# Kernel tuning notes

Measured on AMD Instinct MI355X. Metric: run time of the kernel, lower is better.

## Reference

```python
import jax, jax.numpy as jnp
import numpy as np

MEMORY_LENGTH = 32   # past states remembered
N_TARGETS = 3        # leak sources
T_STEPS = 1000       # duration / dt
DT = 0.1
HIDDEN = 128         # policy MLP hidden width
N_AGENTS = 1024      # vmapped batch of rollouts
IN_DIM = MEMORY_LENGTH * 3 + MEMORY_LENGTH  # flattened x_hist + conc_hist


def setup_inputs() -> dict:
    key = jax.random.key(0)
    k0, k1, k2, k3, k4 = jax.random.split(key, 5)
    target_pos = jax.random.normal(k0, (N_TARGETS, 2), dtype=jnp.float32) * 5.0
    logsigma = jax.random.normal(k1, (N_TARGETS,), dtype=jnp.float32) * 0.5
    x_inits = jax.random.normal(k2, (N_AGENTS, 3), dtype=jnp.float32) * 2.0
    W1 = jax.random.normal(k3, (HIDDEN, IN_DIM), dtype=jnp.float32) / np.sqrt(IN_DIM).astype(np.float32)
    b1 = jnp.zeros((HIDDEN,), dtype=jnp.float32)
    W2 = jax.random.normal(k4, (2, HIDDEN), dtype=jnp.float32) / np.sqrt(HIDDEN).astype(np.float32)
    b2 = jnp.zeros((2,), dtype=jnp.float32)
    return {"target_pos": target_pos, "logsigma": logsigma, "x_inits": x_inits,
            "W1": W1, "b1": b1, "W2": W2, "b2": b2}


def _concentration(x, y, target_pos, sigma):
    # x, y: [N]; target_pos: [nt, 2]; sigma: [nt] -> conc: [N]
    d2 = (x[:, None] - target_pos[None, :, 0]) ** 2 + (y[:, None] - target_pos[None, :, 1]) ** 2
    return ((1.0 / sigma) * jnp.exp(-d2 / sigma)).sum(-1)


def reference(target_pos, logsigma, x_inits, W1, b1, W2, b2):
    sigma = jnp.exp(logsigma)
    N = x_inits.shape[0]
    # initial histories: memory_length copies of the initial state / concentration
    x_hist0 = jnp.tile(x_inits[:, None, :], (1, MEMORY_LENGTH, 1))        # [N, M, 3]
    conc0 = _concentration(x_inits[:, 0], x_inits[:, 1], target_pos, sigma)
    conc_hist0 = jnp.tile(conc0[:, None], (1, MEMORY_LENGTH))             # [N, M]

    def step(carry, _):
        x_hist, conc_hist, x_cur = carry
        # policy MLP on flattened histories -> tanh controls (v, omega)
        feats = jnp.concatenate([x_hist.reshape(N, -1), conc_hist], axis=-1)  # [N, 4M]
        h = jax.nn.relu(feats @ W1.T + b1)
        u = jnp.tanh(h @ W2.T + b2)                                            # [N, 2]
        v, w = u[:, 0], u[:, 1]
        th = x_cur[:, 2]
        # Dubins car dynamics (zero actuation noise)
        x_next = x_cur + DT * jnp.stack([v * jnp.cos(th), v * jnp.sin(th), w], axis=-1)
        # shift histories: drop oldest, insert newest at front
        x_hist = jnp.concatenate([x_next[:, None, :], x_hist[:, :-1, :]], axis=1)
        c = _concentration(x_next[:, 0], x_next[:, 1], target_pos, sigma)
        conc_hist = jnp.concatenate([c[:, None], conc_hist[:, :-1]], axis=1)
        return (x_hist, conc_hist, x_next), (x_next, u)

    _, (traj, ctrl) = jax.lax.scan(step, (x_hist0, conc_hist0, x_inits), None, length=T_STEPS)
    # traj: [T, N, 3], ctrl: [T, N, 2]
    d2 = ((traj[:, :, 0][..., None] - target_pos[None, None, :, 0]) ** 2
          + (traj[:, :, 1][..., None] - target_pos[None, None, :, 1]) ** 2)   # [T, N, nt]
    per_target = (-1.0 / sigma) * jnp.exp(-d2 / sigma)                        # [T, N, nt]
    cost = per_target.mean(axis=(0, 1)).sum() + (ctrl ** 2).mean()
    return cost
```

## Files before the change

kernel.cpp:

```cpp
#include <hip/hip_runtime.h>

#define T_STEPS 1000
#define DT 0.1f
#define HIDDEN 128
#define N_AGENTS 1024

typedef float v2f __attribute__((ext_vector_type(2)));

__device__ __forceinline__ float tanh_fast(float x) {
    float e = __expf(2.0f * x);
    return 1.0f - 2.0f * __builtin_amdgcn_rcpf(e + 1.0f);
}

__device__ __forceinline__ v2f opaque_load8(const float* p) {
    v2f v;
    asm volatile("global_load_dwordx2 %0, %1, off\n\ts_waitcnt vmcnt(0)"
                 : "=v"(v)
                 : "v"((unsigned long long)(uintptr_t)p)
                 : "memory");
    return v;
}

__device__ __forceinline__ float uniformf(float v) {
    return __builtin_bit_cast(float,
        __builtin_amdgcn_readfirstlane(__builtin_bit_cast(int, v)));
}

__device__ __forceinline__ void wave_sum2_dpp(float& a, float& b) {
    asm volatile(
        "s_nop 1\n\t"
        "v_add_f32_dpp %0, %0, %0 row_shr:1 row_mask:0xf bank_mask:0xf bound_ctrl:0\n\t"
        "v_add_f32_dpp %1, %1, %1 row_shr:1 row_mask:0xf bank_mask:0xf bound_ctrl:0\n\t"
        "s_nop 0\n\t"
        "v_add_f32_dpp %0, %0, %0 row_shr:2 row_mask:0xf bank_mask:0xf bound_ctrl:0\n\t"
        "v_add_f32_dpp %1, %1, %1 row_shr:2 row_mask:0xf bank_mask:0xf bound_ctrl:0\n\t"
        "s_nop 0\n\t"
        "v_add_f32_dpp %0, %0, %0 row_shr:4 row_mask:0xf bank_mask:0xf bound_ctrl:0\n\t"
        "v_add_f32_dpp %1, %1, %1 row_shr:4 row_mask:0xf bank_mask:0xf bound_ctrl:0\n\t"
        "s_nop 0\n\t"
        "v_add_f32_dpp %0, %0, %0 row_shr:8 row_mask:0xf bank_mask:0xf bound_ctrl:0\n\t"
        "v_add_f32_dpp %1, %1, %1 row_shr:8 row_mask:0xf bank_mask:0xf bound_ctrl:0\n\t"
        "s_nop 0\n\t"
        "v_add_f32_dpp %0, %0, %0 row_bcast:15 row_mask:0xa bank_mask:0xf bound_ctrl:0\n\t"
        "v_add_f32_dpp %1, %1, %1 row_bcast:15 row_mask:0xa bank_mask:0xf bound_ctrl:0\n\t"
        "s_nop 0\n\t"
        "v_add_f32_dpp %0, %0, %0 row_bcast:31 row_mask:0xc bank_mask:0xf bound_ctrl:0\n\t"
        "v_add_f32_dpp %1, %1, %1 row_bcast:31 row_mask:0xc bank_mask:0xf bound_ctrl:0\n\t"
        "s_nop 1"
        : "+v"(a), "+v"(b));
}

__global__ void pack_kernel(const float* __restrict__ W1,
                            float* __restrict__ pw) {
    const int row = blockIdx.x;
    const int a   = threadIdx.x;
    const float* rp = W1 + row * 128;
    float* out = pw + row * 128;
    out[2*a]          = rp[3*a];
    out[2*a + 1]      = rp[3*a + 1];
    out[64 + 2*a]     = rp[3*a + 2];
    out[64 + 2*a + 1] = rp[96 + a];
}

__global__ __launch_bounds__(128)
__attribute__((amdgpu_waves_per_eu(2, 2)))
void sim_kernel(const float* __restrict__ target_pos,
                const float* __restrict__ logsigma,
                const float* __restrict__ x_inits,
                const float* __restrict__ pw,
                const float* __restrict__ b1,
                const float* __restrict__ W2,
                const float* __restrict__ b2,
                float2* __restrict__ ws) {
    const int agent = blockIdx.x;
    const int tid  = threadIdx.x;
    const int h    = tid >> 6;
    const int lane = tid & 63;
    const int rowA = lane;
    const int rowB = lane + 64;

    __shared__ float2 part1[32][64];
    __shared__ float4 e4buf[16];

    if (h == 0) __builtin_amdgcn_s_setprio(1);

    const float tx0 = uniformf(target_pos[0]), ty0 = uniformf(target_pos[1]);
    const float tx1 = uniformf(target_pos[2]), ty1 = uniformf(target_pos[3]);
    const float tx2 = uniformf(target_pos[4]), ty2 = uniformf(target_pos[5]);
    const float is0 = uniformf(1.0f / expf(logsigma[0]));
    const float is1 = uniformf(1.0f / expf(logsigma[1]));
    const float is2 = uniformf(1.0f / expf(logsigma[2]));

    v2f WxyA[16], WzcA[16], WxyB[16], WzcB[16];
    {
        const float* baseA = pw + rowA * 128;
        const float* baseB = pw + rowB * 128;
        #pragma unroll
        for (int i = 0; i < 16; ++i) {
            WxyA[i] = opaque_load8(baseA + 32 * h + 2 * i);
            WzcA[i] = opaque_load8(baseA + 64 + 32 * h + 2 * i);
            WxyB[i] = opaque_load8(baseB + 32 * h + 2 * i);
            WzcB[i] = opaque_load8(baseB + 64 + 32 * h + 2 * i);
        }
    }
    const float b1A = b1[rowA], b1B = b1[rowB];
    const float w20A = W2[rowA], w20B = W2[rowB];
    const float w21A = W2[HIDDEN + rowA], w21B = W2[HIDDEN + rowB];
    const float b2x = uniformf(b2[0]), b2y = uniformf(b2[1]);

    auto conc = [&](float px, float py) {
        float dx0 = px - tx0, dy0 = py - ty0;
        float dx1 = px - tx1, dy1 = py - ty1;
        float dx2 = px - tx2, dy2 = py - ty2;
        float cc  = is0 * __expf(-(dx0*dx0 + dy0*dy0) * is0);
        cc       += is1 * __expf(-(dx1*dx1 + dy1*dy1) * is1);
        cc       += is2 * __expf(-(dx2*dx2 + dy2*dy2) * is2);
        return cc;
    };

    float x  = uniformf(x_inits[3 * agent]);
    float y  = uniformf(x_inits[3 * agent + 1]);
    float th = uniformf(x_inits[3 * agent + 2]);
    float c  = conc(x, y);

    if (h == 0) {
        v2f RA[16], RB[16];
        {
            v2f exy0 = {x, y}, ezc0 = {th, c};
            v2f aA = {0.f,0.f}, aB = {0.f,0.f};
            #pragma unroll
            for (int k = 15; k >= 0; --k) {
                aA = WxyA[k]*exy0 + aA;  aA = WzcA[k]*ezc0 + aA;
                aB = WxyB[k]*exy0 + aB;  aB = WzcB[k]*ezc0 + aB;
                RA[k] = aA;  RB[k] = aB;
            }
            if (lane == 0) {
                float4 e0 = make_float4(x, y, th, c);
                #pragma unroll
                for (int m = 9; m < 16; ++m) e4buf[m] = e0;
                e4buf[0] = e0;
            }
        }
        __syncthreads();
        float2 pl = part1[0][lane];
        v2f es_xy[4], es_zc[4];
        float S_c = 0.f, S_u = 0.f;

        auto h0_step = [&](int j, int s16) {
            float hA = fmaxf((RA[j].x + RA[j].y) + pl.x + b1A, 0.f);
            float hB = fmaxf((RB[j].x + RB[j].y) + pl.y + b1B, 0.f);
            float r0 = fmaf(w20A, hA, w20B * hB);
            float r1 = fmaf(w21A, hA, w21B * hB);
            wave_sum2_dpp(r0, r1);
            float s0 = __builtin_bit_cast(float,
                __builtin_amdgcn_readlane(__builtin_bit_cast(int, r0), 63));
            float s1 = __builtin_bit_cast(float,
                __builtin_amdgcn_readlane(__builtin_bit_cast(int, r1), 63));
            float v  = tanh_fast(s0 + b2x);
            float wv = tanh_fast(s1 + b2y);
            S_u += v * v + wv * wv;
            float sn = __sinf(th), cs = __cosf(th);
            float dv = DT * v;
            x  = fmaf(dv, cs, x);
            y  = fmaf(dv, sn, y);
            th = fmaf(DT, wv, th);
            c  = conc(x, y);
            S_c += c;
            if (lane == 0) e4buf[(j + 1) & 15] = make_float4(x, y, th, c);
            v2f exy = {x, y}, ezc = {th, c};
            es_xy[j & 3] = exy;  es_zc[j & 3] = ezc;
            #pragma unroll
            for (int k = 0; k < 3; ++k) {
                if (k <= 2 - (j & 3)) {
                    const int m = (j + 1 + k) & 15;
                    RA[m] = WxyA[k]*exy + RA[m];  RA[m] = WzcA[k]*ezc + RA[m];
                    RB[m] = WxyB[k]*exy + RB[m];  RB[m] = WzcB[k]*ezc + RB[m];
                }
            }
            pl = part1[(s16 + j + 1) & 31][lane];
        };
        auto h0_batch = [&](int q) {
            #pragma unroll
            for (int kk = 0; kk < 16; ++kk) {
                #pragma unroll
                for (int i = 0; i < 4; ++i) {
                    if (kk >= 3 - i) {
                        const int m = (4*q + i + 1 + kk) & 15;
                        if (i == 3 && kk >= 12) {
                            RA[m] = WxyA[kk]*es_xy[i];
                            RA[m] = WzcA[kk]*es_zc[i] + RA[m];
                            RB[m] = WxyB[kk]*es_xy[i];
                            RB[m] = WzcB[kk]*es_zc[i] + RB[m];
                        } else {
                            RA[m] = WxyA[kk]*es_xy[i] + RA[m];
                            RA[m] = WzcA[kk]*es_zc[i] + RA[m];
                            RB[m] = WxyB[kk]*es_xy[i] + RB[m];
                            RB[m] = WzcB[kk]*es_zc[i] + RB[m];
                        }
                    }
                }
            }
        };

        #pragma unroll 1
        for (int b = 0; b < 62; ++b) {
            const int s16 = (b & 1) << 4;
            __syncthreads();
            #pragma unroll
            for (int j = 0; j < 4; ++j) h0_step(j, s16);
            h0_batch(0);
            #pragma unroll
            for (int j = 4; j < 8; ++j) h0_step(j, s16);
            h0_batch(1);
            __syncthreads();
            #pragma unroll
            for (int j = 8; j < 12; ++j) h0_step(j, s16);
            h0_batch(2);
            #pragma unroll
            for (int j = 12; j < 16; ++j) h0_step(j, s16);
            h0_batch(3);
        }
        __syncthreads();
        #pragma unroll
        for (int j = 0; j < 4; ++j) h0_step(j, 0);
        h0_batch(0);
        #pragma unroll
        for (int j = 4; j < 8; ++j) h0_step(j, 0);

        if (lane == 0) ws[agent] = make_float2(S_c, S_u);
    } else {
        v2f PA[20], PB[20];
        {
            v2f exy0 = {x, y}, ezc0 = {th, c};
            #pragma unroll
            for (int i = 15; i < 20; ++i) { PA[i] = (v2f){0.f,0.f}; PB[i] = (v2f){0.f,0.f}; }
            v2f aA = {0.f,0.f}, aB = {0.f,0.f};
            #pragma unroll
            for (int k = 15; k >= 1; --k) {
                aA = WxyA[k]*exy0 + aA;  aA = WzcA[k]*ezc0 + aA;
                aB = WxyB[k]*exy0 + aB;  aB = WzcB[k]*ezc0 + aB;
                PA[k-1] = aA;  PB[k-1] = aB;
            }
            v2f fA = WxyA[0]*exy0 + aA;  fA = WzcA[0]*ezc0 + fA;
            v2f fB = WxyB[0]*exy0 + aB;  fB = WzcB[0]*ezc0 + fB;
            float2 full = make_float2(fA.x + fA.y, fB.x + fB.y);
            #pragma unroll
            for (int s = 0; s <= 8; ++s) part1[s][lane] = full;
        }
        __syncthreads();

        auto h1_batch = [&](int n, int b1w) {
            v2f pxy[4], pzc[4];
            #pragma unroll
            for (int i = 0; i < 4; ++i) {
                float4 e = e4buf[(9 + 4*n + i) & 15];
                pxy[i] = (v2f){e.x, e.y};
                pzc[i] = (v2f){e.z, e.w};
            }
            #pragma unroll
            for (int kk = 0; kk < 16; ++kk) {
                #pragma unroll
                for (int i = 0; i < 4; ++i) {
                    const int idx = i + kk;
                    PA[idx] = WxyA[kk]*pxy[i] + PA[idx];
                    PA[idx] = WzcA[kk]*pzc[i] + PA[idx];
                    PB[idx] = WxyB[kk]*pxy[i] + PB[idx];
                    PB[idx] = WzcB[kk]*pzc[i] + PB[idx];
                }
            }
            #pragma unroll
            for (int i = 0; i < 4; ++i) {
                part1[(b1w * 16 + 9 + 4*n + i) & 31][lane] =
                    make_float2(PA[i].x + PA[i].y, PB[i].x + PB[i].y);
            }
            #pragma unroll
            for (int i = 0; i < 16; ++i) { PA[i] = PA[i+4]; PB[i] = PB[i+4]; }
            #pragma unroll
            for (int i = 16; i < 20; ++i) { PA[i] = (v2f){0.f,0.f}; PB[i] = (v2f){0.f,0.f}; }
        };

        #pragma unroll 1
        for (int b = 0; b < 62; ++b) {
            const int b1w = b & 1;
            __syncthreads();
            h1_batch(0, b1w);
            h1_batch(1, b1w);
            __syncthreads();
            h1_batch(2, b1w);
            h1_batch(3, b1w);
        }
        __syncthreads();
    }
}

__global__ void reduce_kernel(const float2* __restrict__ ws,
                              float* __restrict__ out) {
    const int tid = threadIdx.x;
    float sc = 0.f, su = 0.f;
    for (int i = tid; i < N_AGENTS; i += 256) {
        float2 v = ws[i];
        sc += v.x;
        su += v.y;
    }
    #pragma unroll
    for (int off = 32; off > 0; off >>= 1) {
        sc += __shfl_xor(sc, off);
        su += __shfl_xor(su, off);
    }
    __shared__ float2 partw[4];
    int wave = tid >> 6;
    if ((tid & 63) == 0) partw[wave] = make_float2(sc, su);
    __syncthreads();
    if (tid == 0) {
        float SC = partw[0].x + partw[1].x + partw[2].x + partw[3].x;
        float SU = partw[0].y + partw[1].y + partw[2].y + partw[3].y;
        const float invNT  = 1.0f / (float)(N_AGENTS * T_STEPS);
        const float invNT2 = 1.0f / (float)(N_AGENTS * T_STEPS * 2);
        out[0] = -SC * invNT + SU * invNT2;
    }
}

extern "C" void kernel_launch(void* const* d_in, const int* in_sizes, int n_in,
                              void* d_out, int out_size, void* d_ws, size_t ws_size,
                              hipStream_t stream) {
    const float* target_pos = (const float*)d_in[0];
    const float* logsigma   = (const float*)d_in[1];
    const float* x_inits    = (const float*)d_in[2];
    const float* W1         = (const float*)d_in[3];
    const float* b1         = (const float*)d_in[4];
    const float* W2         = (const float*)d_in[5];
    const float* b2         = (const float*)d_in[6];

    float*  pw   = (float*)d_ws;
    float2* sums = (float2*)((char*)d_ws + 64 * 1024);

    pack_kernel<<<HIDDEN, 32, 0, stream>>>(W1, pw);
    sim_kernel<<<N_AGENTS, 128, 0, stream>>>(target_pos, logsigma, x_inits,
                                             pw, b1, W2, b2, sums);
    reduce_kernel<<<1, 256, 0, stream>>>(sums, (float*)d_out);
}
```

Baseline: 632.3 us.

## Merge two-wave producer/consumer split into a single wave per agent

Collapses the two cooperating waves per agent (one stepping dynamics, one precomputing older-history partial sums through LDS with barriers) into one 64-thread wave. That wave holds all W1 columns in registers and interleaves the older-history partial-sum batches between dynamics step groups, using register arrays and double-buffered state vectors. This removes the LDS traffic and __syncthreads barriers on the critical loop. In exchange the serial chain per wave gets longer, since the batch work no longer overlaps, and register pressure roughly doubles (128 v2f weights), which risks spills.

```diff
diff --git a/kernel.cpp b/kernel.cpp
--- a/kernel.cpp
+++ b/kernel.cpp
@@ -62,8 +62,8 @@
     out[64 + 2*a + 1] = rp[96 + a];
 }
 
-__global__ __launch_bounds__(128)
-__attribute__((amdgpu_waves_per_eu(2, 2)))
+__global__ __launch_bounds__(64)
+__attribute__((amdgpu_waves_per_eu(1, 1)))
 void sim_kernel(const float* __restrict__ target_pos,
                 const float* __restrict__ logsigma,
                 const float* __restrict__ x_inits,
@@ -73,16 +73,9 @@
                 const float* __restrict__ b2,
                 float2* __restrict__ ws) {
     const int agent = blockIdx.x;
-    const int tid  = threadIdx.x;
-    const int h    = tid >> 6;
-    const int lane = tid & 63;
+    const int lane  = threadIdx.x;
     const int rowA = lane;
     const int rowB = lane + 64;
-
-    __shared__ float2 part1[32][64];
-    __shared__ float4 e4buf[16];
-
-    if (h == 0) __builtin_amdgcn_s_setprio(1);
 
     const float tx0 = uniformf(target_pos[0]), ty0 = uniformf(target_pos[1]);
     const float tx1 = uniformf(target_pos[2]), ty1 = uniformf(target_pos[3]);
@@ -91,16 +84,16 @@
     const float is1 = uniformf(1.0f / expf(logsigma[1]));
     const float is2 = uniformf(1.0f / expf(logsigma[2]));
 
-    v2f WxyA[16], WzcA[16], WxyB[16], WzcB[16];
+    v2f WxyA[32], WzcA[32], WxyB[32], WzcB[32];
     {
         const float* baseA = pw + rowA * 128;
         const float* baseB = pw + rowB * 128;
         #pragma unroll
-        for (int i = 0; i < 16; ++i) {
-            WxyA[i] = opaque_load8(baseA + 32 * h + 2 * i);
-            WzcA[i] = opaque_load8(baseA + 64 + 32 * h + 2 * i);
-            WxyB[i] = opaque_load8(baseB + 32 * h + 2 * i);
-            WzcB[i] = opaque_load8(baseB + 64 + 32 * h + 2 * i);
+        for (int i = 0; i < 32; ++i) {
+            WxyA[i] = opaque_load8(baseA + 2 * i);
+            WzcA[i] = opaque_load8(baseA + 64 + 2 * i);
+            WxyB[i] = opaque_load8(baseB + 2 * i);
+            WzcB[i] = opaque_load8(baseB + 64 + 2 * i);
         }
     }
     const float b1A = b1[rowA], b1B = b1[rowB];
@@ -123,174 +116,152 @@
     float th = uniformf(x_inits[3 * agent + 2]);
     float c  = conc(x, y);
 
-    if (h == 0) {
-        v2f RA[16], RB[16];
-        {
-            v2f exy0 = {x, y}, ezc0 = {th, c};
-            v2f aA = {0.f,0.f}, aB = {0.f,0.f};
+    v2f RA[16], RB[16];
+    v2f PA[20], PB[20];
+    float plA[16], plB[16];
+    v2f eA_xy[4], eA_zc[4];
+    v2f eB_xy[4], eB_zc[4];
+    float S_c = 0.f, S_u = 0.f;
+
+    {
+        v2f exy0 = {x, y}, ezc0 = {th, c};
+        {   v2f aA = {0.f,0.f}, aB = {0.f,0.f};
             #pragma unroll
             for (int k = 15; k >= 0; --k) {
                 aA = WxyA[k]*exy0 + aA;  aA = WzcA[k]*ezc0 + aA;
                 aB = WxyB[k]*exy0 + aB;  aB = WzcB[k]*ezc0 + aB;
                 RA[k] = aA;  RB[k] = aB;
             }
-            if (lane == 0) {
-                float4 e0 = make_float4(x, y, th, c);
-                #pragma unroll
-                for (int m = 9; m < 16; ++m) e4buf[m] = e0;
-                e4buf[0] = e0;
-            }
-        }
-        __syncthreads();
-        float2 pl = part1[0][lane];
-        v2f es_xy[4], es_zc[4];
-        float S_c = 0.f, S_u = 0.f;
-
-        auto h0_step = [&](int j, int s16) {
-            float hA = fmaxf((RA[j].x + RA[j].y) + pl.x + b1A, 0.f);
-            float hB = fmaxf((RB[j].x + RB[j].y) + pl.y + b1B, 0.f);
-            float r0 = fmaf(w20A, hA, w20B * hB);
-            float r1 = fmaf(w21A, hA, w21B * hB);
-            wave_sum2_dpp(r0, r1);
-            float s0 = __builtin_bit_cast(float,
-                __builtin_amdgcn_readlane(__builtin_bit_cast(int, r0), 63));
-            float s1 = __builtin_bit_cast(float,
-                __builtin_amdgcn_readlane(__builtin_bit_cast(int, r1), 63));
-            float v  = tanh_fast(s0 + b2x);
-            float wv = tanh_fast(s1 + b2y);
-            S_u += v * v + wv * wv;
-            float sn = __sinf(th), cs = __cosf(th);
-            float dv = DT * v;
-            x  = fmaf(dv, cs, x);
-            y  = fmaf(dv, sn, y);
-            th = fmaf(DT, wv, th);
-            c  = conc(x, y);
-            S_c += c;
-            if (lane == 0) e4buf[(j + 1) & 15] = make_float4(x, y, th, c);
-            v2f exy = {x, y}, ezc = {th, c};
-            es_xy[j & 3] = exy;  es_zc[j & 3] = ezc;
-            #pragma unroll
-            for (int k = 0; k < 3; ++k) {
-                if (k <= 2 - (j & 3)) {
-                    const int m = (j + 1 + k) & 15;
-                    RA[m] = WxyA[k]*exy + RA[m];  RA[m] = WzcA[k]*ezc + RA[m];
-                    RB[m] = WxyB[k]*exy + RB[m];  RB[m] = WzcB[k]*ezc + RB[m];
+        }
+        #pragma unroll
+        for (int i = 15; i < 20; ++i) { PA[i] = (v2f){0.f,0.f}; PB[i] = (v2f){0.f,0.f}; }
+        {   v2f aA = {0.f,0.f}, aB = {0.f,0.f};
+            #pragma unroll
+            for (int k = 15; k >= 1; --k) {
+                aA = WxyA[16+k]*exy0 + aA;  aA = WzcA[16+k]*ezc0 + aA;
+                aB = WxyB[16+k]*exy0 + aB;  aB = WzcB[16+k]*ezc0 + aB;
+                PA[k-1] = aA;  PB[k-1] = aB;
+            }
+            v2f fA = WxyA[16]*exy0 + aA;  fA = WzcA[16]*ezc0 + fA;
+            v2f fB = WxyB[16]*exy0 + aB;  fB = WzcB[16]*ezc0 + fB;
+            float fullA = fA.x + fA.y, fullB = fB.x + fB.y;
+            #pragma unroll
+            for (int s = 0; s <= 8; ++s) { plA[s] = fullA; plB[s] = fullB; }
+        }
+        #pragma unroll
+        for (int i = 0; i < 4; ++i) { eB_xy[i] = exy0; eB_zc[i] = ezc0; }
+    }
+
+    auto h1_batch = [&](v2f (&px)[4], v2f (&pz)[4], int n) {
+        #pragma unroll
+        for (int kk = 0; kk < 16; ++kk) {
+            #pragma unroll
+            for (int i = 0; i < 4; ++i) {
+                const int idx = i + kk;
+                if (i == 3 && kk >= 12) {
+                    PA[idx] = WxyA[16+kk]*px[i];
+                    PA[idx] = WzcA[16+kk]*pz[i] + PA[idx];
+                    PB[idx] = WxyB[16+kk]*px[i];
+                    PB[idx] = WzcB[16+kk]*pz[i] + PB[idx];
+                } else {
+                    PA[idx] = WxyA[16+kk]*px[i] + PA[idx];
+                    PA[idx] = WzcA[16+kk]*pz[i] + PA[idx];
+                    PB[idx] = WxyB[16+kk]*px[i] + PB[idx];
+                    PB[idx] = WzcB[16+kk]*pz[i] + PB[idx];
                 }
             }
-            pl = part1[(s16 + j + 1) & 31][lane];
-        };
-        auto h0_batch = [&](int q) {
-            #pragma unroll
-            for (int kk = 0; kk < 16; ++kk) {
-                #pragma unroll
-                for (int i = 0; i < 4; ++i) {
-                    if (kk >= 3 - i) {
-                        const int m = (4*q + i + 1 + kk) & 15;
-                        if (i == 3 && kk >= 12) {
-                            RA[m] = WxyA[kk]*es_xy[i];
-                            RA[m] = WzcA[kk]*es_zc[i] + RA[m];
-                            RB[m] = WxyB[kk]*es_xy[i];
-                            RB[m] = WzcB[kk]*es_zc[i] + RB[m];
-                        } else {
-                            RA[m] = WxyA[kk]*es_xy[i] + RA[m];
-                            RA[m] = WzcA[kk]*es_zc[i] + RA[m];
-                            RB[m] = WxyB[kk]*es_xy[i] + RB[m];
-                            RB[m] = WzcB[kk]*es_zc[i] + RB[m];
-                        }
+        }
+        #pragma unroll
+        for (int i = 0; i < 4; ++i) {
+            plA[(9 + 4*n + i) & 15] = PA[i].x + PA[i].y;
+            plB[(9 + 4*n + i) & 15] = PB[i].x + PB[i].y;
+        }
+        #pragma unroll
+        for (int i = 0; i < 16; ++i) { PA[i] = PA[i+4]; PB[i] = PB[i+4]; }
+    };
+
+    h1_batch(eB_xy, eB_zc, 0);
+
+    auto h0_step = [&](int j, v2f (&bx)[4], v2f (&bz)[4]) {
+        float hA = fmaxf((RA[j & 15].x + RA[j & 15].y) + plA[j & 15] + b1A, 0.f);
+        float hB = fmaxf((RB[j & 15].x + RB[j & 15].y) + plB[j & 15] + b1B, 0.f);
+        float r0 = fmaf(w20A, hA, w20B * hB);
+        float r1 = fmaf(w21A, hA, w21B * hB);
+        wave_sum2_dpp(r0, r1);
+        float s0 = __builtin_bit_cast(float,
+            __builtin_amdgcn_readlane(__builtin_bit_cast(int, r0), 63));
+        float s1 = __builtin_bit_cast(float,
+            __builtin_amdgcn_readlane(__builtin_bit_cast(int, r1), 63));
+        float v  = tanh_fast(s0 + b2x);
+        float wv = tanh_fast(s1 + b2y);
+        S_u += v * v + wv * wv;
+        float sn = __sinf(th), cs = __cosf(th);
+        float dv = DT * v;
+        x  = fmaf(dv, cs, x);
+        y  = fmaf(dv, sn, y);
+        th = fmaf(DT, wv, th);
+        c  = conc(x, y);
+        S_c += c;
+        v2f exy = {x, y}, ezc = {th, c};
+        bx[j & 3] = exy;  bz[j & 3] = ezc;
+        #pragma unroll
+        for (int k = 0; k < 3; ++k) {
+            if (k <= 2 - (j & 3)) {
+                const int m = (j + 1 + k) & 15;
+                RA[m] = WxyA[k]*exy + RA[m];  RA[m] = WzcA[k]*ezc + RA[m];
+                RB[m] = WxyB[k]*exy + RB[m];  RB[m] = WzcB[k]*ezc + RB[m];
+            }
+        }
+    };
+    auto h0_batch = [&](int q, v2f (&bx)[4], v2f (&bz)[4]) {
+        #pragma unroll
+        for (int kk = 0; kk < 16; ++kk) {
+            #pragma unroll
+            for (int i = 0; i < 4; ++i) {
+                if (kk >= 3 - i) {
+                    const int m = (4*q + i + 1 + kk) & 15;
+                    if (i == 3 && kk >= 12) {
+                        RA[m] = WxyA[kk]*bx[i];
+                        RA[m] = WzcA[kk]*bz[i] + RA[m];
+                        RB[m] = WxyB[kk]*bx[i];
+                        RB[m] = WzcB[kk]*bz[i] + RB[m];
+                    } else {
+                        RA[m] = WxyA[kk]*bx[i] + RA[m];
+                        RA[m] = WzcA[kk]*bz[i] + RA[m];
+                        RB[m] = WxyB[kk]*bx[i] + RB[m];
+                        RB[m] = WzcB[kk]*bz[i] + RB[m];
                     }
                 }
             }
-        };
-
-        #pragma unroll 1
-        for (int b = 0; b < 62; ++b) {
-            const int s16 = (b & 1) << 4;
-            __syncthreads();
-            #pragma unroll
-            for (int j = 0; j < 4; ++j) h0_step(j, s16);
-            h0_batch(0);
-            #pragma unroll
-            for (int j = 4; j < 8; ++j) h0_step(j, s16);
-            h0_batch(1);
-            __syncthreads();
-            #pragma unroll
-            for (int j = 8; j < 12; ++j) h0_step(j, s16);
-            h0_batch(2);
-            #pragma unroll
-            for (int j = 12; j < 16; ++j) h0_step(j, s16);
-            h0_batch(3);
-        }
-        __syncthreads();
-        #pragma unroll
-        for (int j = 0; j < 4; ++j) h0_step(j, 0);
-        h0_batch(0);
-        #pragma unroll
-        for (int j = 4; j < 8; ++j) h0_step(j, 0);
-
-        if (lane == 0) ws[agent] = make_float2(S_c, S_u);
-    } else {
-        v2f PA[20], PB[20];
-        {
-            v2f exy0 = {x, y}, ezc0 = {th, c};
-            #pragma unroll
-            for (int i = 15; i < 20; ++i) { PA[i] = (v2f){0.f,0.f}; PB[i] = (v2f){0.f,0.f}; }
-            v2f aA = {0.f,0.f}, aB = {0.f,0.f};
-            #pragma unroll
-            for (int k = 15; k >= 1; --k) {
-                aA = WxyA[k]*exy0 + aA;  aA = WzcA[k]*ezc0 + aA;
-                aB = WxyB[k]*exy0 + aB;  aB = WzcB[k]*ezc0 + aB;
-                PA[k-1] = aA;  PB[k-1] = aB;
-            }
-            v2f fA = WxyA[0]*exy0 + aA;  fA = WzcA[0]*ezc0 + fA;
-            v2f fB = WxyB[0]*exy0 + aB;  fB = WzcB[0]*ezc0 + fB;
-            float2 full = make_float2(fA.x + fA.y, fB.x + fB.y);
-            #pragma unroll
-            for (int s = 0; s <= 8; ++s) part1[s][lane] = full;
-        }
-        __syncthreads();
-
-        auto h1_batch = [&](int n, int b1w) {
-            v2f pxy[4], pzc[4];
-            #pragma unroll
-            for (int i = 0; i < 4; ++i) {
-                float4 e = e4buf[(9 + 4*n + i) & 15];
-                pxy[i] = (v2f){e.x, e.y};
-                pzc[i] = (v2f){e.z, e.w};
-            }
-            #pragma unroll
-            for (int kk = 0; kk < 16; ++kk) {
-                #pragma unroll
-                for (int i = 0; i < 4; ++i) {
-                    const int idx = i + kk;
-                    PA[idx] = WxyA[kk]*pxy[i] + PA[idx];
-                    PA[idx] = WzcA[kk]*pzc[i] + PA[idx];
-                    PB[idx] = WxyB[kk]*pxy[i] + PB[idx];
-                    PB[idx] = WzcB[kk]*pzc[i] + PB[idx];
-                }
-            }
-            #pragma unroll
-            for (int i = 0; i < 4; ++i) {
-                part1[(b1w * 16 + 9 + 4*n + i) & 31][lane] =
-                    make_float2(PA[i].x + PA[i].y, PB[i].x + PB[i].y);
-            }
-            #pragma unroll
-            for (int i = 0; i < 16; ++i) { PA[i] = PA[i+4]; PB[i] = PB[i+4]; }
-            #pragma unroll
-            for (int i = 16; i < 20; ++i) { PA[i] = (v2f){0.f,0.f}; PB[i] = (v2f){0.f,0.f}; }
-        };
-
-        #pragma unroll 1
-        for (int b = 0; b < 62; ++b) {
-            const int b1w = b & 1;
-            __syncthreads();
-            h1_batch(0, b1w);
-            h1_batch(1, b1w);
-            __syncthreads();
-            h1_batch(2, b1w);
-            h1_batch(3, b1w);
-        }
-        __syncthreads();
-    }
+        }
+    };
+
+    #pragma unroll 1
+    for (int b = 0; b < 62; ++b) {
+        h0_step(0, eA_xy, eA_zc);  h0_step(1, eA_xy, eA_zc);
+        h0_step(2, eA_xy, eA_zc);  h0_step(3, eA_xy, eA_zc);
+        h0_batch(0, eA_xy, eA_zc);
+        h1_batch(eB_xy, eB_zc, 1);
+        h0_step(4, eB_xy, eB_zc);  h0_step(5, eB_xy, eB_zc);
+        h0_step(6, eB_xy, eB_zc);  h0_step(7, eB_xy, eB_zc);
+        h0_batch(1, eB_xy, eB_zc);
+        h1_batch(eA_xy, eA_zc, 2);
+        h0_step(8, eA_xy, eA_zc);   h0_step(9, eA_xy, eA_zc);
+        h0_step(10, eA_xy, eA_zc);  h0_step(11, eA_xy, eA_zc);
+        h0_batch(2, eA_xy, eA_zc);
+        h1_batch(eB_xy, eB_zc, 3);
+        h0_step(12, eB_xy, eB_zc);  h0_step(13, eB_xy, eB_zc);
+        h0_step(14, eB_xy, eB_zc);  h0_step(15, eB_xy, eB_zc);
+        h0_batch(3, eB_xy, eB_zc);
+        h1_batch(eA_xy, eA_zc, 0);
+    }
+    h0_step(0, eA_xy, eA_zc);  h0_step(1, eA_xy, eA_zc);
+    h0_step(2, eA_xy, eA_zc);  h0_step(3, eA_xy, eA_zc);
+    h0_batch(0, eA_xy, eA_zc);
+    h0_step(4, eB_xy, eB_zc);  h0_step(5, eB_xy, eB_zc);
+    h0_step(6, eB_xy, eB_zc);  h0_step(7, eB_xy, eB_zc);
+
+    if (lane == 0) ws[agent] = make_float2(S_c, S_u);
 }
 
 __global__ void reduce_kernel(const float2* __restrict__ ws,
@@ -335,7 +306,7 @@
     float2* sums = (float2*)((char*)d_ws + 64 * 1024);
 
     pack_kernel<<<HIDDEN, 32, 0, stream>>>(W1, pw);
-    sim_kernel<<<N_AGENTS, 128, 0, stream>>>(target_pos, logsigma, x_inits,
-                                             pw, b1, W2, b2, sums);
+    sim_kernel<<<N_AGENTS, 64, 0, stream>>>(target_pos, logsigma, x_inits,
+                                            pw, b1, W2, b2, sums);
     reduce_kernel<<<1, 256, 0, stream>>>(sums, (float*)d_out);
 }
```

After: 1.792 ms. 2.83x slower.

## Process two agents per block with weights in AGPRs to interleave serial chains

Applied to the files above, without the earlier changes.

Each block now simulates two agents instead of one. The dependent per-step chains (the DPP reduction, tanh, dynamics and concentration) of the two agents are interleaved, hiding their latency, and the weight reads are amortized over both. Weights move into accumulation registers via v_accvgpr_write/read to make room for the doubled accumulator state, and occupancy is set to one wave per EU. Smaller changes: the DPP reduction is widened to four values without the s_nop padding, sin/cos is computed one step ahead, and history writes are batched. The risks are extra accvgpr read traffic, register pressure, and half as many blocks on a 256-CU part.

```diff
diff --git a/kernel.cpp b/kernel.cpp
--- a/kernel.cpp
+++ b/kernel.cpp
@@ -8,7 +8,7 @@
 typedef float v2f __attribute__((ext_vector_type(2)));
 
 __device__ __forceinline__ float tanh_fast(float x) {
-    float e = __expf(2.0f * x);
+    float e = __builtin_amdgcn_exp2f(x * 0x1.715476p+1f);
     return 1.0f - 2.0f * __builtin_amdgcn_rcpf(e + 1.0f);
 }
 
@@ -21,33 +21,52 @@
     return v;
 }
 
+__device__ __forceinline__ void awrite(float& ax, float& ay, v2f v) {
+    asm("v_accvgpr_write_b32 %0, %2\n\tv_accvgpr_write_b32 %1, %3"
+        : "=a"(ax), "=a"(ay) : "v"(v.x), "v"(v.y));
+}
+__device__ __forceinline__ v2f aread(const float& ax, const float& ay) {
+    float rx, ry;
+    asm("v_accvgpr_read_b32 %0, %2\n\tv_accvgpr_read_b32 %1, %3"
+        : "=v"(rx), "=v"(ry) : "a"(ax), "a"(ay));
+    return (v2f){rx, ry};
+}
+
 __device__ __forceinline__ float uniformf(float v) {
     return __builtin_bit_cast(float,
         __builtin_amdgcn_readfirstlane(__builtin_bit_cast(int, v)));
 }
 
-__device__ __forceinline__ void wave_sum2_dpp(float& a, float& b) {
+__device__ __forceinline__ void wave_sum4_dpp(float& a, float& b,
+                                              float& c, float& d) {
     asm volatile(
         "s_nop 1\n\t"
         "v_add_f32_dpp %0, %0, %0 row_shr:1 row_mask:0xf bank_mask:0xf bound_ctrl:0\n\t"
         "v_add_f32_dpp %1, %1, %1 row_shr:1 row_mask:0xf bank_mask:0xf bound_ctrl:0\n\t"
-        "s_nop 0\n\t"
+        "v_add_f32_dpp %2, %2, %2 row_shr:1 row_mask:0xf bank_mask:0xf bound_ctrl:0\n\t"
+        "v_add_f32_dpp %3, %3, %3 row_shr:1 row_mask:0xf bank_mask:0xf bound_ctrl:0\n\t"
         "v_add_f32_dpp %0, %0, %0 row_shr:2 row_mask:0xf bank_mask:0xf bound_ctrl:0\n\t"
         "v_add_f32_dpp %1, %1, %1 row_shr:2 row_mask:0xf bank_mask:0xf bound_ctrl:0\n\t"
-        "s_nop 0\n\t"
+        "v_add_f32_dpp %2, %2, %2 row_shr:2 row_mask:0xf bank_mask:0xf bound_ctrl:0\n\t"
+        "v_add_f32_dpp %3, %3, %3 row_shr:2 row_mask:0xf bank_mask:0xf bound_ctrl:0\n\t"
         "v_add_f32_dpp %0, %0, %0 row_shr:4 row_mask:0xf bank_mask:0xf bound_ctrl:0\n\t"
         "v_add_f32_dpp %1, %1, %1 row_shr:4 row_mask:0xf bank_mask:0xf bound_ctrl:0\n\t"
-        "s_nop 0\n\t"
+        "v_add_f32_dpp %2, %2, %2 row_shr:4 row_mask:0xf bank_mask:0xf bound_ctrl:0\n\t"
+        "v_add_f32_dpp %3, %3, %3 row_shr:4 row_mask:0xf bank_mask:0xf bound_ctrl:0\n\t"
         "v_add_f32_dpp %0, %0, %0 row_shr:8 row_mask:0xf bank_mask:0xf bound_ctrl:0\n\t"
         "v_add_f32_dpp %1, %1, %1 row_shr:8 row_mask:0xf bank_mask:0xf bound_ctrl:0\n\t"
-        "s_nop 0\n\t"
+        "v_add_f32_dpp %2, %2, %2 row_shr:8 row_mask:0xf bank_mask:0xf bound_ctrl:0\n\t"
+        "v_add_f32_dpp %3, %3, %3 row_shr:8 row_mask:0xf bank_mask:0xf bound_ctrl:0\n\t"
         "v_add_f32_dpp %0, %0, %0 row_bcast:15 row_mask:0xa bank_mask:0xf bound_ctrl:0\n\t"
         "v_add_f32_dpp %1, %1, %1 row_bcast:15 row_mask:0xa bank_mask:0xf bound_ctrl:0\n\t"
-        "s_nop 0\n\t"
+        "v_add_f32_dpp %2, %2, %2 row_bcast:15 row_mask:0xa bank_mask:0xf bound_ctrl:0\n\t"
+        "v_add_f32_dpp %3, %3, %3 row_bcast:15 row_mask:0xa bank_mask:0xf bound_ctrl:0\n\t"
         "v_add_f32_dpp %0, %0, %0 row_bcast:31 row_mask:0xc bank_mask:0xf bound_ctrl:0\n\t"
         "v_add_f32_dpp %1, %1, %1 row_bcast:31 row_mask:0xc bank_mask:0xf bound_ctrl:0\n\t"
+        "v_add_f32_dpp %2, %2, %2 row_bcast:31 row_mask:0xc bank_mask:0xf bound_ctrl:0\n\t"
+        "v_add_f32_dpp %3, %3, %3 row_bcast:31 row_mask:0xc bank_mask:0xf bound_ctrl:0\n\t"
         "s_nop 1"
-        : "+v"(a), "+v"(b));
+        : "+v"(a), "+v"(b), "+v"(c), "+v"(d));
 }
 
 __global__ void pack_kernel(const float* __restrict__ W1,
@@ -63,7 +82,7 @@
 }
 
 __global__ __launch_bounds__(128)
-__attribute__((amdgpu_waves_per_eu(2, 2)))
+__attribute__((amdgpu_waves_per_eu(1, 1)))
 void sim_kernel(const float* __restrict__ target_pos,
                 const float* __restrict__ logsigma,
                 const float* __restrict__ x_inits,
@@ -72,15 +91,15 @@
                 const float* __restrict__ W2,
                 const float* __restrict__ b2,
                 float2* __restrict__ ws) {
-    const int agent = blockIdx.x;
+    const int blk  = blockIdx.x;
     const int tid  = threadIdx.x;
     const int h    = tid >> 6;
     const int lane = tid & 63;
     const int rowA = lane;
     const int rowB = lane + 64;
 
-    __shared__ float2 part1[32][64];
-    __shared__ float4 e4buf[16];
+    __shared__ float2 part1[2][32][64];
+    __shared__ float4 e4buf[2][16];
 
     if (h == 0) __builtin_amdgcn_s_setprio(1);
 
@@ -91,18 +110,24 @@
     const float is1 = uniformf(1.0f / expf(logsigma[1]));
     const float is2 = uniformf(1.0f / expf(logsigma[2]));
 
-    v2f WxyA[16], WzcA[16], WxyB[16], WzcB[16];
+    float WxAx[16], WxAy[16], WzAx[16], WzAy[16];
+    float WxBx[16], WxBy[16], WzBx[16], WzBy[16];
     {
         const float* baseA = pw + rowA * 128;
         const float* baseB = pw + rowB * 128;
         #pragma unroll
         for (int i = 0; i < 16; ++i) {
-            WxyA[i] = opaque_load8(baseA + 32 * h + 2 * i);
-            WzcA[i] = opaque_load8(baseA + 64 + 32 * h + 2 * i);
-            WxyB[i] = opaque_load8(baseB + 32 * h + 2 * i);
-            WzcB[i] = opaque_load8(baseB + 64 + 32 * h + 2 * i);
-        }
-    }
+            awrite(WxAx[i], WxAy[i], opaque_load8(baseA + 32*h + 2*i));
+            awrite(WzAx[i], WzAy[i], opaque_load8(baseA + 64 + 32*h + 2*i));
+            awrite(WxBx[i], WxBy[i], opaque_load8(baseB + 32*h + 2*i));
+            awrite(WzBx[i], WzBy[i], opaque_load8(baseB + 64 + 32*h + 2*i));
+        }
+    }
+    #define WXA(k) aread(WxAx[k], WxAy[k])
+    #define WZA(k) aread(WzAx[k], WzAy[k])
+    #define WXB(k) aread(WxBx[k], WxBy[k])
+    #define WZB(k) aread(WzBx[k], WzBy[k])
+
     const float b1A = b1[rowA], b1B = b1[rowB];
     const float w20A = W2[rowA], w20B = W2[rowB];
     const float w21A = W2[HIDDEN + rowA], w21B = W2[HIDDEN + rowB];
@@ -118,84 +143,140 @@
         return cc;
     };
 
-    float x  = uniformf(x_inits[3 * agent]);
-    float y  = uniformf(x_inits[3 * agent + 1]);
-    float th = uniformf(x_inits[3 * agent + 2]);
-    float c  = conc(x, y);
+    float x[2], y[2], th[2], c[2];
+    #pragma unroll
+    for (int ag = 0; ag < 2; ++ag) {
+        const int agent = 2*blk + ag;
+        x[ag]  = uniformf(x_inits[3*agent]);
+        y[ag]  = uniformf(x_inits[3*agent + 1]);
+        th[ag] = uniformf(x_inits[3*agent + 2]);
+        c[ag]  = conc(x[ag], y[ag]);
+    }
 
     if (h == 0) {
-        v2f RA[16], RB[16];
+        v2f RA[2][16], RB[2][16];
         {
-            v2f exy0 = {x, y}, ezc0 = {th, c};
-            v2f aA = {0.f,0.f}, aB = {0.f,0.f};
+            v2f exy0[2], ezc0[2], aA[2], aB[2];
+            #pragma unroll
+            for (int ag = 0; ag < 2; ++ag) {
+                exy0[ag] = (v2f){x[ag], y[ag]};
+                ezc0[ag] = (v2f){th[ag], c[ag]};
+                aA[ag] = (v2f){0.f,0.f};  aB[ag] = (v2f){0.f,0.f};
+            }
             #pragma unroll
             for (int k = 15; k >= 0; --k) {
-                aA = WxyA[k]*exy0 + aA;  aA = WzcA[k]*ezc0 + aA;
-                aB = WxyB[k]*exy0 + aB;  aB = WzcB[k]*ezc0 + aB;
-                RA[k] = aA;  RB[k] = aB;
+                v2f wxa = WXA(k), wza = WZA(k);
+                v2f wxb = WXB(k), wzb = WZB(k);
+                #pragma unroll
+                for (int ag = 0; ag < 2; ++ag) {
+                    aA[ag] = wxa*exy0[ag] + aA[ag];  aA[ag] = wza*ezc0[ag] + aA[ag];
+                    aB[ag] = wxb*exy0[ag] + aB[ag];  aB[ag] = wzb*ezc0[ag] + aB[ag];
+                    RA[ag][k] = aA[ag];  RB[ag][k] = aB[ag];
+                }
             }
             if (lane == 0) {
-                float4 e0 = make_float4(x, y, th, c);
-                #pragma unroll
-                for (int m = 9; m < 16; ++m) e4buf[m] = e0;
-                e4buf[0] = e0;
-            }
-        }
+                #pragma unroll
+                for (int ag = 0; ag < 2; ++ag) {
+                    float4 e0 = make_float4(x[ag], y[ag], th[ag], c[ag]);
+                    #pragma unroll
+                    for (int m = 9; m < 16; ++m) e4buf[ag][m] = e0;
+                    e4buf[ag][0] = e0;
+                }
+            }
+        }
+        float sn[2], cs[2];
+        #pragma unroll
+        for (int ag = 0; ag < 2; ++ag) { sn[ag] = __sinf(th[ag]); cs[ag] = __cosf(th[ag]); }
         __syncthreads();
-        float2 pl = part1[0][lane];
-        v2f es_xy[4], es_zc[4];
-        float S_c = 0.f, S_u = 0.f;
+        float2 pl[2];
+        #pragma unroll
+        for (int ag = 0; ag < 2; ++ag) pl[ag] = part1[ag][0][lane];
+        v2f es_xy[2][4], es_zc[2][4];
+        float S_c[2] = {0.f, 0.f}, S_u[2] = {0.f, 0.f};
 
         auto h0_step = [&](int j, int s16) {
-            float hA = fmaxf((RA[j].x + RA[j].y) + pl.x + b1A, 0.f);
-            float hB = fmaxf((RB[j].x + RB[j].y) + pl.y + b1B, 0.f);
-            float r0 = fmaf(w20A, hA, w20B * hB);
-            float r1 = fmaf(w21A, hA, w21B * hB);
-            wave_sum2_dpp(r0, r1);
-            float s0 = __builtin_bit_cast(float,
-                __builtin_amdgcn_readlane(__builtin_bit_cast(int, r0), 63));
-            float s1 = __builtin_bit_cast(float,
-                __builtin_amdgcn_readlane(__builtin_bit_cast(int, r1), 63));
-            float v  = tanh_fast(s0 + b2x);
-            float wv = tanh_fast(s1 + b2y);
-            S_u += v * v + wv * wv;
-            float sn = __sinf(th), cs = __cosf(th);
-            float dv = DT * v;
-            x  = fmaf(dv, cs, x);
-            y  = fmaf(dv, sn, y);
-            th = fmaf(DT, wv, th);
-            c  = conc(x, y);
-            S_c += c;
-            if (lane == 0) e4buf[(j + 1) & 15] = make_float4(x, y, th, c);
-            v2f exy = {x, y}, ezc = {th, c};
-            es_xy[j & 3] = exy;  es_zc[j & 3] = ezc;
+            float r0[2], r1[2];
+            #pragma unroll
+            for (int ag = 0; ag < 2; ++ag) {
+                float hA = fmaxf((RA[ag][j].x + RA[ag][j].y) + pl[ag].x + b1A, 0.f);
+                float hB = fmaxf((RB[ag][j].x + RB[ag][j].y) + pl[ag].y + b1B, 0.f);
+                r0[ag] = fmaf(w20A, hA, w20B * hB);
+                r1[ag] = fmaf(w21A, hA, w21B * hB);
+            }
+            wave_sum4_dpp(r0[0], r1[0], r0[1], r1[1]);
+            #pragma unroll
+            for (int ag = 0; ag < 2; ++ag) {
+                float s0 = __builtin_bit_cast(float,
+                    __builtin_amdgcn_readlane(__builtin_bit_cast(int, r0[ag]), 63));
+                float s1 = __builtin_bit_cast(float,
+                    __builtin_amdgcn_readlane(__builtin_bit_cast(int, r1[ag]), 63));
+                float v  = tanh_fast(s0 + b2x);
+                float wv = tanh_fast(s1 + b2y);
+                S_u[ag] += v * v + wv * wv;
+                float dv = DT * v;
+                x[ag]  = fmaf(dv, cs[ag], x[ag]);
+                y[ag]  = fmaf(dv, sn[ag], y[ag]);
+                th[ag] = fmaf(DT, wv, th[ag]);
+                sn[ag] = __sinf(th[ag]);  cs[ag] = __cosf(th[ag]);
+                c[ag]  = conc(x[ag], y[ag]);
+                S_c[ag] += c[ag];
+                es_xy[ag][j & 3] = (v2f){x[ag], y[ag]};
+                es_zc[ag][j & 3] = (v2f){th[ag], c[ag]};
+            }
             #pragma unroll
             for (int k = 0; k < 3; ++k) {
                 if (k <= 2 - (j & 3)) {
                     const int m = (j + 1 + k) & 15;
-                    RA[m] = WxyA[k]*exy + RA[m];  RA[m] = WzcA[k]*ezc + RA[m];
-                    RB[m] = WxyB[k]*exy + RB[m];  RB[m] = WzcB[k]*ezc + RB[m];
-                }
-            }
-            pl = part1[(s16 + j + 1) & 31][lane];
+                    v2f wxa = WXA(k), wza = WZA(k);
+                    v2f wxb = WXB(k), wzb = WZB(k);
+                    #pragma unroll
+                    for (int ag = 0; ag < 2; ++ag) {
+                        RA[ag][m] = wxa*es_xy[ag][j & 3] + RA[ag][m];
+                        RA[ag][m] = wza*es_zc[ag][j & 3] + RA[ag][m];
+                        RB[ag][m] = wxb*es_xy[ag][j & 3] + RB[ag][m];
+                        RB[ag][m] = wzb*es_zc[ag][j & 3] + RB[ag][m];
+                    }
+                }
+            }
+            #pragma unroll
+            for (int ag = 0; ag < 2; ++ag)
+                pl[ag] = part1[ag][(s16 + j + 1) & 31][lane];
+        };
+        auto h0_flush = [&](int g) {
+            if (lane == 0) {
+                #pragma unroll
+                for (int ag = 0; ag < 2; ++ag) {
+                    #pragma unroll
+                    for (int i = 0; i < 4; ++i) {
+                        e4buf[ag][(4*g + 1 + i) & 15] =
+                            make_float4(es_xy[ag][i].x, es_xy[ag][i].y,
+                                        es_zc[ag][i].x, es_zc[ag][i].y);
+                    }
+                }
+            }
         };
         auto h0_batch = [&](int q) {
             #pragma unroll
             for (int kk = 0; kk < 16; ++kk) {
+                v2f wxa = WXA(kk), wza = WZA(kk);
+                v2f wxb = WXB(kk), wzb = WZB(kk);
                 #pragma unroll
                 for (int i = 0; i < 4; ++i) {
                     if (kk >= 3 - i) {
                         const int m = (4*q + i + 1 + kk) & 15;
-                        if (i == 3 && kk >= 12) {
-                            RA[m] = WxyA[kk]*es_xy[i];
-                            RA[m] = WzcA[kk]*es_zc[i] + RA[m];
-                            RB[m] = WxyB[kk]*es_xy[i];
-                            RB[m] = WzcB[kk]*es_zc[i] + RB[m];
-                        } else {
-                            RA[m] = WxyA[kk]*es_xy[i] + RA[m];
-                            RA[m] = WzcA[kk]*es_zc[i] + RA[m];
-                            RB[m] = WxyB[kk]*es_xy[i] + RB[m];
-                            RB[m] = WzcB[kk]*es_zc[i] + RB[m];
+                        #pragma unroll
+                        for (int ag = 0; ag < 2; ++ag) {
+                            if (i == 3 && kk >= 12) {
+                                RA[ag][m] = wxa*es_xy[ag][i];
+                                RA[ag][m] = wza*es_zc[ag][i] + RA[ag][m];
+                                RB[ag][m] = wxb*es_xy[ag][i];
+                                RB[ag][m] = wzb*es_zc[ag][i] + RB[ag][m];
+                            } else {
+                                RA[ag][m] = wxa*es_xy[ag][i] + RA[ag][m];
+                                RA[ag][m] = wza*es_zc[ag][i] + RA[ag][m];
+                                RB[ag][m] = wxb*es_xy[ag][i] + RB[ag][m];
+                                RB[ag][m] = wzb*es_zc[ag][i] + RB[ag][m];
+                            }
                         }
                     }
                 }
@@ -206,77 +287,121 @@
         for (int b = 0; b < 62; ++b) {
             const int s16 = (b & 1) << 4;
             __syncthreads();
-            #pragma unroll
-            for (int j = 0; j < 4; ++j) h0_step(j, s16);
+            h0_step(0, s16);  h0_step(1, s16);
+            h0_step(2, s16);  h0_step(3, s16);
+            h0_flush(0);
             h0_batch(0);
-            #pragma unroll
-            for (int j = 4; j < 8; ++j) h0_step(j, s16);
+            h0_step(4, s16);  h0_step(5, s16);
+            h0_step(6, s16);  h0_step(7, s16);
+            h0_flush(1);
             h0_batch(1);
             __syncthreads();
-            #pragma unroll
-            for (int j = 8; j < 12; ++j) h0_step(j, s16);
+            h0_step(8, s16);   h0_step(9, s16);
+            h0_step(10, s16);  h0_step(11, s16);
+            h0_flush(2);
             h0_batch(2);
-            #pragma unroll
-            for (int j = 12; j < 16; ++j) h0_step(j, s16);
+            h0_step(12, s16);  h0_step(13, s16);
+            h0_step(14, s16);  h0_step(15, s16);
+            h0_flush(3);
             h0_batch(3);
         }
         __syncthreads();
-        #pragma unroll
-        for (int j = 0; j < 4; ++j) h0_step(j, 0);
+        h0_step(0, 0);  h0_step(1, 0);
+        h0_step(2, 0);  h0_step(3, 0);
+        h0_flush(0);
         h0_batch(0);
-        #pragma unroll
-        for (int j = 4; j < 8; ++j) h0_step(j, 0);
-
-        if (lane == 0) ws[agent] = make_float2(S_c, S_u);
+        h0_step(4, 0);  h0_step(5, 0);
+        h0_step(6, 0);  h0_step(7, 0);
+
+        if (lane == 0) {
+            ws[2*blk]     = make_float2(S_c[0], S_u[0]);
+            ws[2*blk + 1] = make_float2(S_c[1], S_u[1]);
+        }
     } else {
-        v2f PA[20], PB[20];
+        v2f PA[2][20], PB[2][20];
         {
-            v2f exy0 = {x, y}, ezc0 = {th, c};
-            #pragma unroll
-            for (int i = 15; i < 20; ++i) { PA[i] = (v2f){0.f,0.f}; PB[i] = (v2f){0.f,0.f}; }
-            v2f aA = {0.f,0.f}, aB = {0.f,0.f};
+            v2f exy0[2], ezc0[2], aA[2], aB[2];
+            #pragma unroll
+            for (int ag = 0; ag < 2; ++ag) {
+                exy0[ag] = (v2f){x[ag], y[ag]};
+                ezc0[ag] = (v2f){th[ag], c[ag]};
+                aA[ag] = (v2f){0.f,0.f};  aB[ag] = (v2f){0.f,0.f};
+                #pragma unroll
+                for (int i = 15; i < 20; ++i) {
+                    PA[ag][i] = (v2f){0.f,0.f};  PB[ag][i] = (v2f){0.f,0.f};
+                }
+            }
             #pragma unroll
             for (int k = 15; k >= 1; --k) {
-                aA = WxyA[k]*exy0 + aA;  aA = WzcA[k]*ezc0 + aA;
-                aB = WxyB[k]*exy0 + aB;  aB = WzcB[k]*ezc0 + aB;
-                PA[k-1] = aA;  PB[k-1] = aB;
-            }
-            v2f fA = WxyA[0]*exy0 + aA;  fA = WzcA[0]*ezc0 + fA;
-            v2f fB = WxyB[0]*exy0 + aB;  fB = WzcB[0]*ezc0 + fB;
-            float2 full = make_float2(fA.x + fA.y, fB.x + fB.y);
-            #pragma unroll
-            for (int s = 0; s <= 8; ++s) part1[s][lane] = full;
+                v2f wxa = WXA(k), wza = WZA(k);
+                v2f wxb = WXB(k), wzb = WZB(k);
+                #pragma unroll
+                for (int ag = 0; ag < 2; ++ag) {
+                    aA[ag] = wxa*exy0[ag] + aA[ag];  aA[ag] = wza*ezc0[ag] + aA[ag];
+                    aB[ag] = wxb*exy0[ag] + aB[ag];  aB[ag] = wzb*ezc0[ag] + aB[ag];
+                    PA[ag][k-1] = aA[ag];  PB[ag][k-1] = aB[ag];
+                }
+            }
+            v2f wxa0 = WXA(0), wza0 = WZA(0);
+            v2f wxb0 = WXB(0), wzb0 = WZB(0);
+            #pragma unroll
+            for (int ag = 0; ag < 2; ++ag) {
+                v2f fA = wxa0*exy0[ag] + aA[ag];  fA = wza0*ezc0[ag] + fA;
+                v2f fB = wxb0*exy0[ag] + aB[ag];  fB = wzb0*ezc0[ag] + fB;
+                float2 full = make_float2(fA.x + fA.y, fB.x + fB.y);
+                #pragma unroll
+                for (int s = 0; s <= 8; ++s) part1[ag][s][lane] = full;
+            }
         }
         __syncthreads();
 
         auto h1_batch = [&](int n, int b1w) {
-            v2f pxy[4], pzc[4];
-            #pragma unroll
-            for (int i = 0; i < 4; ++i) {
-                float4 e = e4buf[(9 + 4*n + i) & 15];
-                pxy[i] = (v2f){e.x, e.y};
-                pzc[i] = (v2f){e.z, e.w};
+            v2f pxy[2][4], pzc[2][4];
+            #pragma unroll
+            for (int ag = 0; ag < 2; ++ag) {
+                #pragma unroll
+                for (int i = 0; i < 4; ++i) {
+                    float4 e = e4buf[ag][(9 + 4*n + i) & 15];
+                    pxy[ag][i] = (v2f){e.x, e.y};
+                    pzc[ag][i] = (v2f){e.z, e.w};
+                }
             }
             #pragma unroll
             for (int kk = 0; kk < 16; ++kk) {
+                v2f wxa = WXA(kk), wza = WZA(kk);
+                v2f wxb = WXB(kk), wzb = WZB(kk);
                 #pragma unroll
                 for (int i = 0; i < 4; ++i) {
                     const int idx = i + kk;
-                    PA[idx] = WxyA[kk]*pxy[i] + PA[idx];
-                    PA[idx] = WzcA[kk]*pzc[i] + PA[idx];
-                    PB[idx] = WxyB[kk]*pxy[i] + PB[idx];
-                    PB[idx] = WzcB[kk]*pzc[i] + PB[idx];
-                }
-            }
-            #pragma unroll
-            for (int i = 0; i < 4; ++i) {
-                part1[(b1w * 16 + 9 + 4*n + i) & 31][lane] =
-                    make_float2(PA[i].x + PA[i].y, PB[i].x + PB[i].y);
-            }
-            #pragma unroll
-            for (int i = 0; i < 16; ++i) { PA[i] = PA[i+4]; PB[i] = PB[i+4]; }
-            #pragma unroll
-            for (int i = 16; i < 20; ++i) { PA[i] = (v2f){0.f,0.f}; PB[i] = (v2f){0.f,0.f}; }
+                    #pragma unroll
+                    for (int ag = 0; ag < 2; ++ag) {
+                        if (i == 3 && kk >= 12) {
+                            PA[ag][idx] = wxa*pxy[ag][i];
+                            PA[ag][idx] = wza*pzc[ag][i] + PA[ag][idx];
+                            PB[ag][idx] = wxb*pxy[ag][i];
+                            PB[ag][idx] = wzb*pzc[ag][i] + PB[ag][idx];
+                        } else {
+                            PA[ag][idx] = wxa*pxy[ag][i] + PA[ag][idx];
+                            PA[ag][idx] = wza*pzc[ag][i] + PA[ag][idx];
+                            PB[ag][idx] = wxb*pxy[ag][i] + PB[ag][idx];
+                            PB[ag][idx] = wzb*pzc[ag][i] + PB[ag][idx];
+                        }
+                    }
+                }
+            }
+            #pragma unroll
+            for (int ag = 0; ag < 2; ++ag) {
+                #pragma unroll
+                for (int i = 0; i < 4; ++i) {
+                    part1[ag][(b1w * 16 + 9 + 4*n + i) & 31][lane] =
+                        make_float2(PA[ag][i].x + PA[ag][i].y,
+                                    PB[ag][i].x + PB[ag][i].y);
+                }
+                #pragma unroll
+                for (int i = 0; i < 16; ++i) {
+                    PA[ag][i] = PA[ag][i+4];  PB[ag][i] = PB[ag][i+4];
+                }
+            }
         };
 
         #pragma unroll 1
@@ -335,7 +460,7 @@
     float2* sums = (float2*)((char*)d_ws + 64 * 1024);
 
     pack_kernel<<<HIDDEN, 32, 0, stream>>>(W1, pw);
-    sim_kernel<<<N_AGENTS, 128, 0, stream>>>(target_pos, logsigma, x_inits,
-                                             pw, b1, W2, b2, sums);
+    sim_kernel<<<N_AGENTS / 2, 128, 0, stream>>>(target_pos, logsigma, x_inits,
+                                                 pw, b1, W2, b2, sums);
     reduce_kernel<<<1, 256, 0, stream>>>(sums, (float*)d_out);
 }
```

Measured after the change: 1.232 ms. 94.8% more time.
